# Kernel tuning notes

Measured on AMD Instinct MI355X. Metric: run time of the kernel, lower is better.

## Reference

```python
import jax, jax.numpy as jnp
import numpy as np

HIDDEN = 1024
HEADS = 16
HEAD_DIM = HIDDEN // HEADS  # 64


def setup_inputs() -> dict:
    key = jax.random.key(0)
    kx, kqkv, ko = jax.random.split(key, 3)
    x = jax.random.normal(kx, (2, 2048, HIDDEN), dtype=jnp.float32)
    # Xavier-uniform init like the torch module; torch Linear weight is [out, in]
    lim_qkv = float(np.sqrt(6.0 / (HIDDEN + 3 * HIDDEN)))
    qkv_w = jax.random.uniform(kqkv, (3 * HIDDEN, HIDDEN), minval=-lim_qkv, maxval=lim_qkv, dtype=jnp.float32)
    qkv_b = jnp.zeros((3 * HIDDEN,), dtype=jnp.float32)
    lim_o = float(np.sqrt(6.0 / (HIDDEN + HIDDEN)))
    o_w = jax.random.uniform(ko, (HIDDEN, HIDDEN), minval=-lim_o, maxval=lim_o, dtype=jnp.float32)
    o_b = jnp.zeros((HIDDEN,), dtype=jnp.float32)
    return {"x": x, "qkv_w": qkv_w, "qkv_b": qkv_b, "o_w": o_w, "o_b": o_b}


def reference(x, qkv_w, qkv_b, o_w, o_b):
    B, S, D = x.shape
    H, Dh = HEADS, HEAD_DIM
    # qkv projection (torch Linear: x @ W.T + b) -> [B, S, 3*D]
    qkv = jnp.einsum('bsd,ed->bse', x, qkv_w) + qkv_b
    # reshape to [B, H, S, 3*Dh] then split into q, k, v
    qkv = qkv.reshape(B, S, H, 3 * Dh).transpose(0, 2, 1, 3)
    q, k, v = jnp.split(qkv, 3, axis=-1)  # each [B, H, S, Dh]
    # scaled dot-product attention, materializing full [B, H, S, S] scores
    logits = jnp.einsum('bhqd,bhkd->bhqk', q, k) / jnp.sqrt(jnp.asarray(Dh, x.dtype))
    attn = jax.nn.softmax(logits, axis=-1)
    values = jnp.einsum('bhqk,bhkd->bhqd', attn, v)
    # merge heads -> [B, S, D], then output projection
    values = values.transpose(0, 2, 1, 3).reshape(B, S, D)
    return jnp.einsum('bsd,ed->bse', values, o_w) + o_b
```

## Files before the change

kernel.cpp:

```cpp
#include <hip/hip_runtime.h>
#include <hip/hip_bf16.h>

#define BDIM 2
#define SEQ  2048
#define HID  1024
#define NH   16
#define HD   64
#define MROWS (BDIM * SEQ)
#define QKVN  (3 * HID)

typedef __attribute__((ext_vector_type(8))) short s8b;
typedef __attribute__((ext_vector_type(4))) float f4;

__device__ __forceinline__ unsigned f2bf(float f) {
    unsigned u = __builtin_bit_cast(unsigned, f);
    return (u + 0x7FFFu + ((u >> 16) & 1u)) >> 16;
}
__device__ __forceinline__ float bf2f(unsigned h) {
    return __builtin_bit_cast(float, h << 16);
}

__global__ __launch_bounds__(256) void split_hi_lo(
    const float* __restrict__ src, unsigned short* __restrict__ hi,
    unsigned short* __restrict__ lo, int n8)
{
    const int i = blockIdx.x * 256 + threadIdx.x;
    if (i >= n8) return;
    const float4* s = (const float4*)src + 2 * (size_t)i;
    float4 a = s[0], b = s[1];
    const float v[8] = {a.x, a.y, a.z, a.w, b.x, b.y, b.z, b.w};
    unsigned hu[8], lu[8];
#pragma unroll
    for (int j = 0; j < 8; ++j) {
        hu[j] = f2bf(v[j]);
        lu[j] = f2bf(v[j] - bf2f(hu[j]));
    }
    uint4 hv = {hu[0] | (hu[1] << 16), hu[2] | (hu[3] << 16),
                hu[4] | (hu[5] << 16), hu[6] | (hu[7] << 16)};
    uint4 lv = {lu[0] | (lu[1] << 16), lu[2] | (lu[3] << 16),
                lu[4] | (lu[5] << 16), lu[6] | (lu[7] << 16)};
    *((uint4*)hi + i) = hv;
    *((uint4*)lo + i) = lv;
}

template <int OUTBF>
__global__ __launch_bounds__(256)
__attribute__((amdgpu_waves_per_eu(2, 2)))
void gemm_split(
    const unsigned short* __restrict__ Ah, const unsigned short* __restrict__ Al,
    const unsigned short* __restrict__ Wh, const unsigned short* __restrict__ Wl,
    const float* __restrict__ bias, void* __restrict__ Cout, int N, int K)
{
    const int t   = threadIdx.x;
    const int l   = t & 63;
    const int l15 = t & 15;
    const int lg  = (t >> 4) & 3;
    const int w   = t >> 6;
    const int wr  = w >> 1, wc = w & 1;
    const int bm  = blockIdx.y * 128, bn = blockIdx.x * 128;

    __shared__ unsigned short SB[2][4][128 * 32];

    f4 acc[4][4];
#pragma unroll
    for (int i = 0; i < 4; ++i)
#pragma unroll
        for (int j = 0; j < 4; ++j) acc[i][j] = (f4){0.f, 0.f, 0.f, 0.f};

    const unsigned short* plane_src = (w == 0) ? Ah : (w == 1) ? Al
                                    : (w == 2) ? Wh : Wl;
    const int rb0 = (w < 2) ? bm : bn;
    const int gsw = ((l & 3) ^ ((l >> 2) & 3)) * 8;

    auto stage = [&](int buf, int k0) {
        const unsigned short* gp =
            plane_src + (size_t)(rb0 + (l >> 2)) * K + k0 + gsw;
        unsigned short* lb = &SB[buf][w][0];
#pragma unroll
        for (int c = 0; c < 8; ++c)
            __builtin_amdgcn_global_load_lds(
                (const __attribute__((address_space(1))) void*)(gp + (size_t)(c * 16) * K),
                (__attribute__((address_space(3))) void*)(lb + c * 512),
                16, 0, 0);
    };

    const int ksw = ((lg ^ (l15 & 3)) & 3) << 3;

    stage(0, 0);
    __syncthreads();

    int cur = 0;
    const int nsteps = K >> 5;
    for (int step = 0; step < nsteps; ++step) {
        if (step + 1 < nsteps) stage(cur ^ 1, (step + 1) << 5);

        const unsigned short* base = &SB[cur][0][0];
        s8b bh[4], bl[4];
#pragma unroll
        for (int nt = 0; nt < 4; ++nt) {
            const int ro = (wc * 64 + nt * 16 + l15) * 32 + ksw;
            bh[nt] = *(const s8b*)(base + 2 * 4096 + ro);
            bl[nt] = *(const s8b*)(base + 3 * 4096 + ro);
        }
#pragma unroll
        for (int mt = 0; mt < 4; ++mt) {
            const int ro = (wr * 64 + mt * 16 + l15) * 32 + ksw;
            s8b ah = *(const s8b*)(base + ro);
            s8b al = *(const s8b*)(base + 4096 + ro);
#pragma unroll
            for (int nt = 0; nt < 4; ++nt) {
                acc[mt][nt] = __builtin_amdgcn_mfma_f32_16x16x32_bf16(ah, bh[nt], acc[mt][nt], 0, 0, 0);
                acc[mt][nt] = __builtin_amdgcn_mfma_f32_16x16x32_bf16(ah, bl[nt], acc[mt][nt], 0, 0, 0);
                acc[mt][nt] = __builtin_amdgcn_mfma_f32_16x16x32_bf16(al, bh[nt], acc[mt][nt], 0, 0, 0);
            }
        }
        __syncthreads();
        cur ^= 1;
    }

    float bv[4];
#pragma unroll
    for (int nt = 0; nt < 4; ++nt) bv[nt] = bias[bn + wc * 64 + nt * 16 + l15];

#pragma unroll
    for (int mt = 0; mt < 4; ++mt)
#pragma unroll
        for (int i = 0; i < 4; ++i) {
            const int m = bm + wr * 64 + mt * 16 + lg * 4 + i;
#pragma unroll
            for (int nt = 0; nt < 4; ++nt) {
                const int n = bn + wc * 64 + nt * 16 + l15;
                const float v = acc[mt][nt][i] + bv[nt];
                if (OUTBF)
                    ((unsigned short*)Cout)[(size_t)m * N + n] = (unsigned short)f2bf(v);
                else
                    ((float*)Cout)[(size_t)m * N + n] = v;
            }
        }
}

__device__ __forceinline__ int sw_off(int row, int colbyte) {
    return row * 128 + (colbyte ^ ((((row & 7) ^ (row >> 3)) & 7) << 4));
}

__global__ __launch_bounds__(256) void attn_fwd_mfma(
    const unsigned short* __restrict__ qkv,
    unsigned short* __restrict__ att_hi, unsigned short* __restrict__ att_lo)
{
    const int t   = threadIdx.x;
    const int w   = t >> 6;
    const int l   = t & 63;
    const int l15 = l & 15;
    const int lg  = l >> 4;

    const int bh = blockIdx.y;
    const int b  = bh >> 4;
    const int h  = bh & 15;
    const int q0 = blockIdx.x * 64;

    __shared__ unsigned short Ks[64 * 64];
    __shared__ unsigned short Vt[64 * 64];
    __shared__ unsigned short Ps[64 * 64];

    const unsigned short* base = qkv + (size_t)b * SEQ * QKVN + h * (3 * HD);

    s8b qf[2];
    {
        const unsigned short* qrow = base + (size_t)(q0 + w * 16 + l15) * QKVN;
        qf[0] = *(const s8b*)(qrow + lg * 8);
        qf[1] = *(const s8b*)(qrow + 32 + lg * 8);
    }

    float m_run[4], l_run[4];
    f4 oacc[4];
#pragma unroll
    for (int i = 0; i < 4; ++i) {
        m_run[i] = -1e30f;
        l_run[i] = 0.f;
        oacc[i]  = (f4){0.f, 0.f, 0.f, 0.f};
    }

    for (int kt = 0; kt < SEQ; kt += 64) {
        __syncthreads();

#pragma unroll
        for (int rep = 0; rep < 2; ++rep) {
            const int idx = t + rep * 256;
            const int row = idx >> 3;
            const int gg  = idx & 7;
            const unsigned short* src = base + (size_t)(kt + row) * QKVN + HD + gg * 8;
            uint4 kg = *(const uint4*)src;
            *(uint4*)((char*)Ks + sw_off(row, gg * 16)) = kg;

            s8b v8 = *(const s8b*)(src + HD);
#pragma unroll
            for (int j = 0; j < 8; ++j)
                *(unsigned short*)((char*)Vt + sw_off(gg * 8 + j, row * 2)) =
                    (unsigned short)v8[j];
        }
        __syncthreads();

        f4 sacc[4];
#pragma unroll
        for (int nt = 0; nt < 4; ++nt) sacc[nt] = (f4){0.f, 0.f, 0.f, 0.f};
#pragma unroll
        for (int kc = 0; kc < 2; ++kc) {
            const int colb = kc * 64 + lg * 16;
#pragma unroll
            for (int nt = 0; nt < 4; ++nt) {
                s8b kf = *(const s8b*)((const char*)Ks + sw_off(nt * 16 + l15, colb));
                sacc[nt] = __builtin_amdgcn_mfma_f32_16x16x32_bf16(qf[kc], kf, sacc[nt], 0, 0, 0);
            }
        }
#pragma unroll
        for (int nt = 0; nt < 4; ++nt)
#pragma unroll
            for (int i = 0; i < 4; ++i) sacc[nt][i] *= 0.125f;

        float mt4[4];
#pragma unroll
        for (int i = 0; i < 4; ++i)
            mt4[i] = fmaxf(fmaxf(sacc[0][i], sacc[1][i]), fmaxf(sacc[2][i], sacc[3][i]));
#pragma unroll
        for (int s = 1; s <= 8; s <<= 1)
#pragma unroll
            for (int i = 0; i < 4; ++i)
                mt4[i] = fmaxf(mt4[i], __shfl_xor(mt4[i], s));

        float corr[4], rs[4];
#pragma unroll
        for (int i = 0; i < 4; ++i) {
            const float mn = fmaxf(m_run[i], mt4[i]);
            corr[i]  = __expf(m_run[i] - mn);
            m_run[i] = mn;
            rs[i]    = 0.f;
        }

        const int rowbase = w * 16 + lg * 4;
#pragma unroll
        for (int nt = 0; nt < 4; ++nt) {
#pragma unroll
            for (int i = 0; i < 4; ++i) {
                const float p = __expf(sacc[nt][i] - m_run[i]);
                rs[i] += p;
                *(unsigned short*)((char*)Ps + sw_off(rowbase + i, (nt * 16 + l15) * 2)) =
                    (unsigned short)f2bf(p);
            }
        }
#pragma unroll
        for (int s = 1; s <= 8; s <<= 1)
#pragma unroll
            for (int i = 0; i < 4; ++i)
                rs[i] += __shfl_xor(rs[i], s);
#pragma unroll
        for (int i = 0; i < 4; ++i)
            l_run[i] = l_run[i] * corr[i] + rs[i];
#pragma unroll
        for (int nt = 0; nt < 4; ++nt)
#pragma unroll
            for (int i = 0; i < 4; ++i)
                oacc[nt][i] *= corr[i];

#pragma unroll
        for (int kk = 0; kk < 2; ++kk) {
            const int colb = kk * 64 + lg * 16;
            s8b pf = *(const s8b*)((const char*)Ps + sw_off(w * 16 + l15, colb));
#pragma unroll
            for (int nt = 0; nt < 4; ++nt) {
                s8b vf = *(const s8b*)((const char*)Vt + sw_off(nt * 16 + l15, colb));
                oacc[nt] = __builtin_amdgcn_mfma_f32_16x16x32_bf16(pf, vf, oacc[nt], 0, 0, 0);
            }
        }
    }

    float inv[4];
#pragma unroll
    for (int i = 0; i < 4; ++i) inv[i] = 1.f / l_run[i];
#pragma unroll
    for (int i = 0; i < 4; ++i) {
        const size_t rowb = (size_t)(b * SEQ + q0 + w * 16 + lg * 4 + i) * HID + h * HD + l15;
#pragma unroll
        for (int nt = 0; nt < 4; ++nt) {
            const float v = oacc[nt][i] * inv[i];
            const unsigned hu = f2bf(v);
            const unsigned lu = f2bf(v - bf2f(hu));
            att_hi[rowb + nt * 16] = (unsigned short)hu;
            att_lo[rowb + nt * 16] = (unsigned short)lu;
        }
    }
}

extern "C" void kernel_launch(void* const* d_in, const int* in_sizes, int n_in,
                              void* d_out, int out_size, void* d_ws, size_t ws_size,
                              hipStream_t stream) {
    const float* x     = (const float*)d_in[0];
    const float* qkv_w = (const float*)d_in[1];
    const float* qkv_b = (const float*)d_in[2];
    const float* o_w   = (const float*)d_in[3];
    const float* o_b   = (const float*)d_in[4];
    float* out = (float*)d_out;

    char* ws = (char*)d_ws;
    unsigned short* qkv_bf = (unsigned short*)ws;                      ws += (size_t)MROWS * QKVN * 2;
    unsigned short* wh     = (unsigned short*)ws;                      ws += (size_t)QKVN * HID * 2;
    unsigned short* wl     = (unsigned short*)ws;                      ws += (size_t)QKVN * HID * 2;
    unsigned short* owh    = (unsigned short*)ws;                      ws += (size_t)HID * HID * 2;
    unsigned short* owl    = (unsigned short*)ws;                      ws += (size_t)HID * HID * 2;
    unsigned short* xh     = (unsigned short*)ws;                      ws += (size_t)MROWS * HID * 2;
    unsigned short* xl     = (unsigned short*)ws;
    unsigned short* att_hi = xh;
    unsigned short* att_lo = xl;

    split_hi_lo<<<(MROWS * HID / 8) / 256, 256, 0, stream>>>(x, xh, xl, MROWS * HID / 8);
    split_hi_lo<<<(QKVN * HID / 8) / 256, 256, 0, stream>>>(qkv_w, wh, wl, QKVN * HID / 8);
    split_hi_lo<<<(HID * HID / 8) / 256, 256, 0, stream>>>(o_w, owh, owl, HID * HID / 8);

    gemm_split<1><<<dim3(QKVN / 128, MROWS / 128), 256, 0, stream>>>(
        xh, xl, wh, wl, qkv_b, qkv_bf, QKVN, HID);

    attn_fwd_mfma<<<dim3(SEQ / 64, BDIM * NH), 256, 0, stream>>>(qkv_bf, att_hi, att_lo);

    gemm_split<0><<<dim3(HID / 128, MROWS / 128), 256, 0, stream>>>(
        att_hi, att_lo, owh, owl, o_b, out, HID, HID);

    (void)in_sizes; (void)n_in; (void)out_size; (void)ws_size;
}
```

Measured before the change: 340.3 us.

## Pre-transpose V, enlarge attention query tile, use exp2 and lazy rescaling

Adds a separate kernel that writes V transposed to workspace, so the attention loop loads K and V^T tiles with plain vector copies instead of scattered per-element LDS writes. The attention block grows to 512 threads covering 128 queries, so each K/V tile is reused across twice as many queries. Softmax now uses exp2 with the log2(e) factor folded into the scale, and skips the output and sum rescale when no row maximum grew anywhere in the wave. This costs an extra launch and a global write/read of V^T, and the larger blocks halve the grid size.

```diff
diff --git a/kernel.cpp b/kernel.cpp
--- a/kernel.cpp
+++ b/kernel.cpp
@@ -8,6 +8,7 @@
 #define HD   64
 #define MROWS (BDIM * SEQ)
 #define QKVN  (3 * HID)
+#define QBLK 128
 
 typedef __attribute__((ext_vector_type(8))) short s8b;
 typedef __attribute__((ext_vector_type(4))) float f4;
@@ -143,8 +144,40 @@
     return row * 128 + (colbyte ^ ((((row & 7) ^ (row >> 3)) & 7) << 4));
 }
 
-__global__ __launch_bounds__(256) void attn_fwd_mfma(
+__global__ __launch_bounds__(256) void transpose_v(
+    const unsigned short* __restrict__ qkv, unsigned short* __restrict__ vt)
+{
+    const int bh = blockIdx.y;
+    const int b  = bh >> 4, h = bh & 15;
+    const int s0 = blockIdx.x * 64;
+    const int t  = threadIdx.x;
+
+    __shared__ unsigned short T[64 * 64];
+
+#pragma unroll
+    for (int rep = 0; rep < 2; ++rep) {
+        const int idx = t + rep * 256;
+        const int srow = idx >> 3, gg = idx & 7;
+        uint4 v = *(const uint4*)(qkv + (size_t)(b * SEQ + s0 + srow) * QKVN
+                                  + h * (3 * HD) + 2 * HD + gg * 8);
+        *(uint4*)((char*)T + sw_off(srow, gg * 16)) = v;
+    }
+    __syncthreads();
+#pragma unroll
+    for (int rep = 0; rep < 2; ++rep) {
+        const int idx = t + rep * 256;
+        const int drow = idx >> 3, gg = idx & 7;
+        unsigned short tmp[8];
+#pragma unroll
+        for (int j = 0; j < 8; ++j)
+            tmp[j] = *(const unsigned short*)((const char*)T + sw_off(gg * 8 + j, drow * 2));
+        *(uint4*)(vt + ((size_t)bh * 64 + drow) * SEQ + s0 + gg * 8) = *(const uint4*)tmp;
+    }
+}
+
+__global__ __launch_bounds__(512) void attn_fwd_mfma(
     const unsigned short* __restrict__ qkv,
+    const unsigned short* __restrict__ vt,
     unsigned short* __restrict__ att_hi, unsigned short* __restrict__ att_lo)
 {
     const int t   = threadIdx.x;
@@ -156,13 +189,14 @@
     const int bh = blockIdx.y;
     const int b  = bh >> 4;
     const int h  = bh & 15;
-    const int q0 = blockIdx.x * 64;
+    const int q0 = blockIdx.x * QBLK;
 
     __shared__ unsigned short Ks[64 * 64];
     __shared__ unsigned short Vt[64 * 64];
-    __shared__ unsigned short Ps[64 * 64];
-
-    const unsigned short* base = qkv + (size_t)b * SEQ * QKVN + h * (3 * HD);
+    __shared__ unsigned short Ps[QBLK * 64];
+
+    const unsigned short* base  = qkv + (size_t)b * SEQ * QKVN + h * (3 * HD);
+    const unsigned short* vbase = vt + (size_t)bh * 64 * SEQ;
 
     s8b qf[2];
     {
@@ -180,24 +214,16 @@
         oacc[i]  = (f4){0.f, 0.f, 0.f, 0.f};
     }
 
+    const int srow = t >> 3;
+    const int sgg  = t & 7;
+
     for (int kt = 0; kt < SEQ; kt += 64) {
         __syncthreads();
 
-#pragma unroll
-        for (int rep = 0; rep < 2; ++rep) {
-            const int idx = t + rep * 256;
-            const int row = idx >> 3;
-            const int gg  = idx & 7;
-            const unsigned short* src = base + (size_t)(kt + row) * QKVN + HD + gg * 8;
-            uint4 kg = *(const uint4*)src;
-            *(uint4*)((char*)Ks + sw_off(row, gg * 16)) = kg;
-
-            s8b v8 = *(const s8b*)(src + HD);
-#pragma unroll
-            for (int j = 0; j < 8; ++j)
-                *(unsigned short*)((char*)Vt + sw_off(gg * 8 + j, row * 2)) =
-                    (unsigned short)v8[j];
-        }
+        uint4 kg = *(const uint4*)(base + (size_t)(kt + srow) * QKVN + HD + sgg * 8);
+        *(uint4*)((char*)Ks + sw_off(srow, sgg * 16)) = kg;
+        uint4 vg = *(const uint4*)(vbase + (size_t)srow * SEQ + kt + sgg * 8);
+        *(uint4*)((char*)Vt + sw_off(srow, sgg * 16)) = vg;
         __syncthreads();
 
         f4 sacc[4];
@@ -212,10 +238,11 @@
                 sacc[nt] = __builtin_amdgcn_mfma_f32_16x16x32_bf16(qf[kc], kf, sacc[nt], 0, 0, 0);
             }
         }
+        const float SCL = 0.125f * 1.44269504088896f;
 #pragma unroll
         for (int nt = 0; nt < 4; ++nt)
 #pragma unroll
-            for (int i = 0; i < 4; ++i) sacc[nt][i] *= 0.125f;
+            for (int i = 0; i < 4; ++i) sacc[nt][i] *= SCL;
 
         float mt4[4];
 #pragma unroll
@@ -227,21 +254,27 @@
             for (int i = 0; i < 4; ++i)
                 mt4[i] = fmaxf(mt4[i], __shfl_xor(mt4[i], s));
 
-        float corr[4], rs[4];
-#pragma unroll
-        for (int i = 0; i < 4; ++i) {
-            const float mn = fmaxf(m_run[i], mt4[i]);
-            corr[i]  = __expf(m_run[i] - mn);
-            m_run[i] = mn;
-            rs[i]    = 0.f;
-        }
-
+        bool grew = (mt4[0] > m_run[0]) | (mt4[1] > m_run[1]) |
+                    (mt4[2] > m_run[2]) | (mt4[3] > m_run[3]);
+        if (__any(grew)) {
+#pragma unroll
+            for (int i = 0; i < 4; ++i) {
+                const float mn  = fmaxf(m_run[i], mt4[i]);
+                const float cor = exp2f(m_run[i] - mn);
+                m_run[i] = mn;
+                l_run[i] *= cor;
+#pragma unroll
+                for (int nt = 0; nt < 4; ++nt) oacc[nt][i] *= cor;
+            }
+        }
+
+        float rs[4] = {0.f, 0.f, 0.f, 0.f};
         const int rowbase = w * 16 + lg * 4;
 #pragma unroll
         for (int nt = 0; nt < 4; ++nt) {
 #pragma unroll
             for (int i = 0; i < 4; ++i) {
-                const float p = __expf(sacc[nt][i] - m_run[i]);
+                const float p = exp2f(sacc[nt][i] - m_run[i]);
                 rs[i] += p;
                 *(unsigned short*)((char*)Ps + sw_off(rowbase + i, (nt * 16 + l15) * 2)) =
                     (unsigned short)f2bf(p);
@@ -253,13 +286,7 @@
             for (int i = 0; i < 4; ++i)
                 rs[i] += __shfl_xor(rs[i], s);
 #pragma unroll
-        for (int i = 0; i < 4; ++i)
-            l_run[i] = l_run[i] * corr[i] + rs[i];
-#pragma unroll
-        for (int nt = 0; nt < 4; ++nt)
-#pragma unroll
-            for (int i = 0; i < 4; ++i)
-                oacc[nt][i] *= corr[i];
+        for (int i = 0; i < 4; ++i) l_run[i] += rs[i];
 
 #pragma unroll
         for (int kk = 0; kk < 2; ++kk) {
@@ -301,13 +328,14 @@
     float* out = (float*)d_out;
 
     char* ws = (char*)d_ws;
-    unsigned short* qkv_bf = (unsigned short*)ws;                      ws += (size_t)MROWS * QKVN * 2;
-    unsigned short* wh     = (unsigned short*)ws;                      ws += (size_t)QKVN * HID * 2;
-    unsigned short* wl     = (unsigned short*)ws;                      ws += (size_t)QKVN * HID * 2;
-    unsigned short* owh    = (unsigned short*)ws;                      ws += (size_t)HID * HID * 2;
-    unsigned short* owl    = (unsigned short*)ws;                      ws += (size_t)HID * HID * 2;
-    unsigned short* xh     = (unsigned short*)ws;                      ws += (size_t)MROWS * HID * 2;
-    unsigned short* xl     = (unsigned short*)ws;
+    unsigned short* qkv_bf = (unsigned short*)ws;   ws += (size_t)MROWS * QKVN * 2;
+    unsigned short* wh     = (unsigned short*)ws;   ws += (size_t)QKVN * HID * 2;
+    unsigned short* wl     = (unsigned short*)ws;   ws += (size_t)QKVN * HID * 2;
+    unsigned short* owh    = (unsigned short*)ws;   ws += (size_t)HID * HID * 2;
+    unsigned short* owl    = (unsigned short*)ws;   ws += (size_t)HID * HID * 2;
+    unsigned short* xh     = (unsigned short*)ws;   ws += (size_t)MROWS * HID * 2;
+    unsigned short* xl     = (unsigned short*)ws;   ws += (size_t)MROWS * HID * 2;
+    unsigned short* vt     = (unsigned short*)ws;
     unsigned short* att_hi = xh;
     unsigned short* att_lo = xl;
 
@@ -318,7 +346,10 @@
     gemm_split<1><<<dim3(QKVN / 128, MROWS / 128), 256, 0, stream>>>(
         xh, xl, wh, wl, qkv_b, qkv_bf, QKVN, HID);
 
-    attn_fwd_mfma<<<dim3(SEQ / 64, BDIM * NH), 256, 0, stream>>>(qkv_bf, att_hi, att_lo);
+    transpose_v<<<dim3(SEQ / 64, BDIM * NH), 256, 0, stream>>>(qkv_bf, vt);
+
+    attn_fwd_mfma<<<dim3(SEQ / QBLK, BDIM * NH), 512, 0, stream>>>(
+        qkv_bf, vt, att_hi, att_lo);
 
     gemm_split<0><<<dim3(HID / 128, MROWS / 128), 256, 0, stream>>>(
         att_hi, att_lo, owh, owl, o_b, out, HID, HID);
```

Result: faster. 319.1 us (-6.2%).
